# Performance work log

Measured on AMD Instinct MI355X. Metric: run time of the kernel, lower is better.

## Reference

```python
import jax, jax.numpy as jnp
import numpy as np

B, T, L, W = 4, 4096, 64, 8          # batch, text len, media tokens, max_window_per_audio
DIM, DIM_A, H, DH = 2048, 1024, 8, 64
INNER = H * DH
LN_EPS = 1e-5


def setup_inputs() -> dict:
    key = jax.random.key(0)
    ks = jax.random.split(key, 8)
    x = jax.random.normal(ks[0], (B, T, DIM), jnp.float32)
    media = jax.random.normal(ks[1], (B, L, 1, DIM_A), jnp.float32)
    media_mask = jax.random.uniform(ks[2], (B, L, 1)) > 0.1
    # sparse media markers (~8 per row); ensure at least one per row
    media_locations = (jax.random.uniform(ks[3], (B, T)) < (8.0 / T)).astype(jnp.int32)
    media_locations = media_locations.at[:, 0].set(1)
    Wq = jax.random.normal(ks[4], (DIM, INNER), jnp.float32) / np.sqrt(DIM).astype(np.float32)
    Wkv = jax.random.normal(ks[5], (DIM_A, 2 * INNER), jnp.float32) / np.sqrt(DIM_A).astype(np.float32)
    Wout = jax.random.normal(ks[6], (INNER, DIM), jnp.float32) / np.sqrt(INNER).astype(np.float32)
    gamma = jnp.ones((DIM,), jnp.float32)
    beta = jnp.zeros((DIM,), jnp.float32)
    return dict(x=x, media=media, media_mask=media_mask, media_locations=media_locations,
                Wq=Wq, Wkv=Wkv, Wout=Wout, gamma=gamma, beta=beta)


def reference(x, media, media_mask, media_locations, Wq, Wkv, Wout, gamma, beta):
    scale = DH ** -0.5
    # LayerNorm (biased variance, like torch)
    mu = x.mean(-1, keepdims=True)
    var = x.var(-1, keepdims=True)
    xn = (x - mu) * jax.lax.rsqrt(var + LN_EPS) * gamma + beta
    # projections
    q = (xn @ Wq).reshape(B, T, H, DH).transpose(0, 2, 1, 3) * scale   # [B,h,T,dh]
    kv = media.reshape(B, L, DIM_A) @ Wkv
    k, v = jnp.split(kv, 2, axis=-1)
    k = k.reshape(B, L, H, DH).transpose(0, 2, 1, 3)                   # [B,h,L,dh]
    v = v.reshape(B, L, H, DH).transpose(0, 2, 1, 3)
    sim = jnp.einsum('bhid,bhjd->bhij', q, k)                          # [B,h,T,L]
    big = jnp.finfo(sim.dtype).max
    # media validity mask
    mm = media_mask.reshape(B, 1, 1, L)
    sim = jnp.where(mm, sim, -big)
    # few-shot window mask (only_attend_immediate_media=False):
    # token t attends windows [0, max(#media at <=t, 1) * W)
    cum = jnp.cumsum((media_locations != 0).astype(jnp.int32), axis=1)  # [B,T]
    end = jnp.maximum(cum, 1) * W                                       # [B,T]
    fsm = jnp.arange(L)[None, None, :] < end[:, :, None]                # [B,T,L]
    sim = jnp.where(fsm[:, None], sim, -big)
    sim = sim - jax.lax.stop_gradient(sim.max(-1, keepdims=True))
    attn = jax.nn.softmax(sim, axis=-1)
    out = jnp.einsum('bhij,bhjd->bhid', attn, v)                        # [B,h,T,dh]
    out = out.transpose(0, 2, 1, 3).reshape(B, T, INNER)
    return out @ Wout
```

## Files before the change

kernel.cpp:

```cpp
#include <hip/hip_runtime.h>
#include <float.h>

typedef __bf16 bf16;
typedef __bf16 bf16x8 __attribute__((ext_vector_type(8)));
typedef float f32x4 __attribute__((ext_vector_type(4)));

#define GAS __attribute__((address_space(1)))
#define LAS __attribute__((address_space(3)))

__device__ __forceinline__ void gload_lds16(const void* g, void* l) {
  __builtin_amdgcn_global_load_lds((const GAS unsigned int*)g, (LAS unsigned int*)l, 16, 0, 0);
}

template <int OUT_BF16, int BN>
__global__ __launch_bounds__(512, 2) void gemm_pipe(
    const bf16* __restrict__ A, const bf16* __restrict__ Bt,
    void* __restrict__ Cv, int M, int N, int K) {
  constexpr int NR = BN / 64;
  __shared__ __align__(16) bf16 Abuf[4][256 * 32];
  __shared__ __align__(16) bf16 Bbuf[4][BN * 32];
  const int tid = threadIdx.x, lane = tid & 63, w = tid >> 6;
  const int wr = w >> 2, wc = w & 3;
  const int g = lane >> 4, fr = lane & 15;

  const int gx = gridDim.x;
  const int nwg = gx * gridDim.y;
  int lid = blockIdx.y * gx + blockIdx.x;
  {
    const int qq = nwg >> 3, rr = nwg & 7;
    const int xcd = lid & 7, pos = lid >> 3;
    lid = (xcd < rr ? xcd * (qq + 1) : rr * (qq + 1) + (xcd - rr) * qq) + pos;
  }
  const int bx = lid % gx, by = lid / gx;
  const size_t m0 = (size_t)by * 256, n0 = (size_t)bx * BN;

  const int nt = K >> 5;
  const int srow = w * 16 + (lane >> 2);
  const int sdslot = lane & 3;

  auto stageA = [&](int t) {
    const int q = t & 3;
    const int kt = t << 5;
#pragma unroll
    for (int c = 0; c < 2; ++c) {
      const int r = c * 128 + srow;
      const int ss = sdslot ^ ((r >> 1) & 3);
      gload_lds16(A + (m0 + r) * (size_t)K + kt + ss * 8,
                  &Abuf[q][c * 4096 + w * 512]);
    }
  };
  auto stageB = [&](int t) {
    const int q = t & 3;
    const int kt = t << 5;
#pragma unroll
    for (int c = 0; c < BN / 128; ++c) {
      const int r = c * 128 + srow;
      const int ss = sdslot ^ ((r >> 1) & 3);
      gload_lds16(Bt + (n0 + r) * (size_t)K + kt + ss * 8,
                  &Bbuf[q][c * 4096 + w * 512]);
    }
  };
  auto rdA = [&](int q, int mi) {
    const int r = wr * 128 + mi * 16 + fr;
    return *(const bf16x8*)&Abuf[q][r * 32 + ((g ^ ((r >> 1) & 3)) << 3)];
  };
  auto rdB = [&](int q, int ni) {
    const int r = wc * (BN / 4) + ni * 16 + fr;
    return *(const bf16x8*)&Bbuf[q][r * 32 + ((g ^ ((r >> 1) & 3)) << 3)];
  };

  f32x4 acc[8][NR] = {};

#pragma unroll
  for (int t = 0; t < 4; ++t) {
    stageA(t);
    stageB(t);
  }

  const int body = nt - 4;
  for (int t = 0; t < body; ++t) {
    const int q = t & 3;
    if constexpr (BN == 256)
      asm volatile("s_waitcnt vmcnt(12)" ::: "memory");
    else
      asm volatile("s_waitcnt vmcnt(9)" ::: "memory");
    __builtin_amdgcn_s_barrier();
    __builtin_amdgcn_sched_barrier(0);

    bf16x8 bv[NR], av0[4];
#pragma unroll
    for (int ni = 0; ni < NR; ++ni) bv[ni] = rdB(q, ni);
#pragma unroll
    for (int mi = 0; mi < 4; ++mi) av0[mi] = rdA(q, mi);
    __builtin_amdgcn_s_setprio(1);
#pragma unroll
    for (int mi = 0; mi < 4; ++mi)
#pragma unroll
      for (int ni = 0; ni < NR; ++ni)
        acc[mi][ni] = __builtin_amdgcn_mfma_f32_16x16x32_bf16(
            av0[mi], bv[ni], acc[mi][ni], 0, 0, 0);
    __builtin_amdgcn_s_setprio(0);
    __builtin_amdgcn_s_barrier();
    __builtin_amdgcn_sched_barrier(0);
    stageB(t + 4);

    bf16x8 av1[4];
#pragma unroll
    for (int mi = 0; mi < 4; ++mi) av1[mi] = rdA(q, 4 + mi);
    __builtin_amdgcn_s_setprio(1);
#pragma unroll
    for (int mi = 0; mi < 4; ++mi)
#pragma unroll
      for (int ni = 0; ni < NR; ++ni)
        acc[4 + mi][ni] = __builtin_amdgcn_mfma_f32_16x16x32_bf16(
            av1[mi], bv[ni], acc[4 + mi][ni], 0, 0, 0);
    __builtin_amdgcn_s_setprio(0);
    __builtin_amdgcn_s_barrier();
    __builtin_amdgcn_sched_barrier(0);
    stageA(t + 4);
  }

  asm volatile("s_waitcnt vmcnt(0)" ::: "memory");
  __builtin_amdgcn_s_barrier();
  __builtin_amdgcn_sched_barrier(0);
  for (int t = body; t < nt; ++t) {
    const int q = t & 3;
    bf16x8 bv[NR];
#pragma unroll
    for (int ni = 0; ni < NR; ++ni) bv[ni] = rdB(q, ni);
#pragma unroll
    for (int mh = 0; mh < 2; ++mh) {
      bf16x8 av[4];
#pragma unroll
      for (int mi = 0; mi < 4; ++mi) av[mi] = rdA(q, mh * 4 + mi);
#pragma unroll
      for (int mi = 0; mi < 4; ++mi)
#pragma unroll
        for (int ni = 0; ni < NR; ++ni)
          acc[mh * 4 + mi][ni] = __builtin_amdgcn_mfma_f32_16x16x32_bf16(
              av[mi], bv[ni], acc[mh * 4 + mi][ni], 0, 0, 0);
    }
  }

#pragma unroll
  for (int mi = 0; mi < 8; ++mi)
#pragma unroll
    for (int ni = 0; ni < NR; ++ni)
#pragma unroll
      for (int rg = 0; rg < 4; ++rg) {
        const size_t row = m0 + wr * 128 + mi * 16 + g * 4 + rg;
        const size_t col = n0 + wc * (BN / 4) + ni * 16 + fr;
        if (OUT_BF16)
          ((bf16*)Cv)[row * (size_t)N + col] = (bf16)acc[mi][ni][rg];
        else
          ((float*)Cv)[row * (size_t)N + col] = acc[mi][ni][rg];
      }
}

template <int OUT_BF16>
__global__ __launch_bounds__(256, 2) void gemm_bt(
    const bf16* __restrict__ A, const bf16* __restrict__ Bt,
    void* __restrict__ Cv, int M, int N, int K) {
  __shared__ bf16 As[128 * 32];
  __shared__ bf16 Bs[128 * 32];
  const int tid = threadIdx.x;
  const int lane = tid & 63, w = tid >> 6;
  const int wr = w >> 1, wc = w & 1;

  const int gx = gridDim.x;
  const int nwg = gx * gridDim.y;
  int lid = blockIdx.y * gx + blockIdx.x;
  {
    const int qq = nwg >> 3, rr = nwg & 7;
    const int xcd = lid & 7, pos = lid >> 3;
    lid = (xcd < rr ? xcd * (qq + 1) : rr * (qq + 1) + (xcd - rr) * qq) + pos;
  }
  const int bx = lid % gx, by = lid / gx;
  const size_t m0 = (size_t)by * 128, n0 = (size_t)bx * 128;

  const int srow = lane >> 2, sslot = lane & 3;
  const int g = lane >> 4, fr = lane & 15;

  f32x4 acc[4][4] = {};

  for (int kt = 0; kt < K; kt += 32) {
    __syncthreads();
#pragma unroll
    for (int j = 0; j < 2; ++j) {
      const int c = 2 * w + j;
      const int r = c * 16 + srow;
      const int ks = (sslot ^ (r & 3)) << 3;
      gload_lds16(A + (m0 + r) * K + kt + ks, &As[c * 512]);
      gload_lds16(Bt + (n0 + r) * K + kt + ks, &Bs[c * 512]);
    }
    __syncthreads();
    bf16x8 av[4], bv[4];
#pragma unroll
    for (int mi = 0; mi < 4; ++mi) {
      const int r = wr * 64 + mi * 16 + fr;
      av[mi] = *(const bf16x8*)&As[r * 32 + ((g ^ (r & 3)) << 3)];
    }
#pragma unroll
    for (int ni = 0; ni < 4; ++ni) {
      const int r = wc * 64 + ni * 16 + fr;
      bv[ni] = *(const bf16x8*)&Bs[r * 32 + ((g ^ (r & 3)) << 3)];
    }
#pragma unroll
    for (int mi = 0; mi < 4; ++mi)
#pragma unroll
      for (int ni = 0; ni < 4; ++ni)
        acc[mi][ni] = __builtin_amdgcn_mfma_f32_16x16x32_bf16(
            av[mi], bv[ni], acc[mi][ni], 0, 0, 0);
  }

#pragma unroll
  for (int mi = 0; mi < 4; ++mi)
#pragma unroll
    for (int ni = 0; ni < 4; ++ni)
#pragma unroll
      for (int rg = 0; rg < 4; ++rg) {
        const size_t row = m0 + wr * 64 + mi * 16 + g * 4 + rg;
        const size_t col = n0 + wc * 64 + ni * 16 + fr;
        if (OUT_BF16)
          ((bf16*)Cv)[row * (size_t)N + col] = (bf16)acc[mi][ni][rg];
        else
          ((float*)Cv)[row * (size_t)N + col] = acc[mi][ni][rg];
      }
}

__device__ __forceinline__ void transp64(const float* __restrict__ src,
                                         bf16* __restrict__ dst, int R, int C,
                                         float scale, int tile, float* lds) {
  const int tilesC = C >> 6;
  const int tr = tile / tilesC, tc = tile % tilesC;
  const int r0 = tr << 6, c0 = tc << 6;
  const int tid = threadIdx.x;
  const int lr = tid >> 6, lc = tid & 63;
#pragma unroll
  for (int j = 0; j < 16; ++j) {
    const int r = j * 4 + lr;
    lds[r * 65 + lc] = src[(size_t)(r0 + r) * C + c0 + lc];
  }
  __syncthreads();
#pragma unroll
  for (int j = 0; j < 16; ++j) {
    const int rr = j * 4 + lr;
    dst[(size_t)(c0 + rr) * R + r0 + lc] = (bf16)(lds[lc * 65 + rr] * scale);
  }
}

__global__ __launch_bounds__(256) void prep_all(
    const float* __restrict__ x, const float* __restrict__ gamma,
    const float* __restrict__ beta, bf16* __restrict__ xn,
    const float* __restrict__ Wq, bf16* __restrict__ wqT,
    const float* __restrict__ Wkv, bf16* __restrict__ wkvT,
    const float* __restrict__ Wout, bf16* __restrict__ woT,
    const float* __restrict__ media, bf16* __restrict__ medb,
    const int* __restrict__ mloc, int* __restrict__ endw,
    const unsigned char* __restrict__ mraw, int* __restrict__ mk) {
  __shared__ float shf[64 * 65];
  const int blk = blockIdx.x, tid = threadIdx.x;

  if (blk < 16384) {
    const size_t base = (size_t)blk * 2048 + tid * 8;
    f32x4 v0 = *(const f32x4*)(x + base);
    f32x4 v1 = *(const f32x4*)(x + base + 4);
    float s = 0.f, q2 = 0.f;
#pragma unroll
    for (int j = 0; j < 4; ++j) {
      s += v0[j] + v1[j];
      q2 += v0[j] * v0[j] + v1[j] * v1[j];
    }
    for (int off = 32; off > 0; off >>= 1) {
      s += __shfl_down(s, off);
      q2 += __shfl_down(q2, off);
    }
    const int lane = tid & 63, wv = tid >> 6;
    if (lane == 0) { shf[wv] = s; shf[4 + wv] = q2; }
    __syncthreads();
    s = shf[0] + shf[1] + shf[2] + shf[3];
    q2 = shf[4] + shf[5] + shf[6] + shf[7];
    const float mu = s * (1.f / 2048.f);
    const float var = q2 * (1.f / 2048.f) - mu * mu;
    const float rs = rsqrtf(var + 1e-5f);
    f32x4 g0 = *(const f32x4*)(gamma + tid * 8);
    f32x4 g1 = *(const f32x4*)(gamma + tid * 8 + 4);
    f32x4 b0 = *(const f32x4*)(beta + tid * 8);
    f32x4 b1 = *(const f32x4*)(beta + tid * 8 + 4);
    bf16x8 o;
#pragma unroll
    for (int j = 0; j < 4; ++j) {
      o[j] = (bf16)((v0[j] - mu) * rs * g0[j] + b0[j]);
      o[4 + j] = (bf16)((v1[j] - mu) * rs * g1[j] + b1[j]);
    }
    *(bf16x8*)(xn + base) = o;
  } else if (blk < 16640) {
    transp64(Wq, wqT, 2048, 512, 0.125f, blk - 16384, shf);
  } else if (blk < 16896) {
    transp64(Wkv, wkvT, 1024, 1024, 1.f, blk - 16640, shf);
  } else if (blk < 17152) {
    transp64(Wout, woT, 512, 2048, 1.f, blk - 16896, shf);
  } else if (blk < 18176) {
    const int i = (blk - 17152) * 256 + tid;
    medb[i] = (bf16)media[i];
  } else if (blk < 18180) {
    int* part = (int*)shf;
    const int b = blk - 18176;
    int loc[16];
    int s = 0;
    const int base = b * 4096 + tid * 16;
#pragma unroll
    for (int j = 0; j < 16; ++j) {
      loc[j] = (mloc[base + j] != 0) ? 1 : 0;
      s += loc[j];
    }
    part[tid] = s;
    __syncthreads();
    for (int off = 1; off < 256; off <<= 1) {
      int v = (tid >= off) ? part[tid - off] : 0;
      __syncthreads();
      part[tid] += v;
      __syncthreads();
    }
    int c = (tid > 0) ? part[tid - 1] : 0;
#pragma unroll
    for (int j = 0; j < 16; ++j) {
      c += loc[j];
      int e = (c > 1 ? c : 1) << 3;
      endw[base + j] = e > 64 ? 64 : e;
    }
  } else {
    int* isbool = (int*)shf;
    if (tid == 0) *isbool = 0;
    __syncthreads();
    const unsigned char v = mraw[tid];
    if ((tid & 3) != 0 && v != 0) atomicOr(isbool, 1);
    __syncthreads();
    mk[tid] = (*isbool) ? (int)mraw[tid] : ((const int*)mraw)[tid];
  }
}

__global__ __launch_bounds__(256, 2) void attn_kernel(
    const bf16* __restrict__ q, const bf16* __restrict__ kv,
    const int* __restrict__ mk, const int* __restrict__ endw,
    bf16* __restrict__ ao) {
  __shared__ bf16 Ks[64 * 64], Vs[64 * 64], Ps[64 * 64];
  __shared__ int mks[64];
  const int tid = threadIdx.x, lane = tid & 63, w = tid >> 6;
  const int b = blockIdx.z, h = blockIdx.y, t0 = blockIdx.x * 64;

#pragma unroll
  for (int s0 = 0; s0 < 2; ++s0) {
    const int sidx = s0 * 256 + tid;
    const int r = sidx >> 3, sl = sidx & 7;
    *(bf16x8*)&Ks[r * 64 + ((sl ^ (r & 7)) << 3)] =
        *(const bf16x8*)&kv[(size_t)(b * 64 + r) * 1024 + h * 64 + sl * 8];
    bf16x8 vv =
        *(const bf16x8*)&kv[(size_t)(b * 64 + r) * 1024 + 512 + h * 64 + sl * 8];
#pragma unroll
    for (int j = 0; j < 8; ++j) {
      const int dh = sl * 8 + j;
      Vs[dh * 64 + ((((r >> 3) ^ (dh & 7)) << 3) | (r & 7))] = vv[j];
    }
  }
  if (tid < 64) mks[tid] = mk[b * 64 + tid];
  __syncthreads();

  const int g = lane >> 4, fr = lane & 15;
  bf16x8 aq[2];
#pragma unroll
  for (int kg = 0; kg < 2; ++kg)
    aq[kg] = *(const bf16x8*)&q[(size_t)(b * 4096 + t0 + w * 16 + fr) * 512 +
                                h * 64 + kg * 32 + g * 8];
  f32x4 sacc[4] = {};
#pragma unroll
  for (int kg = 0; kg < 2; ++kg)
#pragma unroll
    for (int ni = 0; ni < 4; ++ni) {
      const int r = ni * 16 + fr;
      bf16x8 bk = *(const bf16x8*)&Ks[r * 64 + (((kg * 4 + g) ^ (r & 7)) << 3)];
      sacc[ni] = __builtin_amdgcn_mfma_f32_16x16x32_bf16(aq[kg], bk, sacc[ni],
                                                         0, 0, 0);
    }

  const int4 ev4 = *(const int4*)&endw[b * 4096 + t0 + w * 16 + g * 4];
  const int ev[4] = {ev4.x, ev4.y, ev4.z, ev4.w};
  float p[4][4];
#pragma unroll
  for (int ni = 0; ni < 4; ++ni) {
    const int l = ni * 16 + fr;
    const bool mv = (mks[l] != 0);
#pragma unroll
    for (int rg = 0; rg < 4; ++rg)
      p[ni][rg] = (mv && (l < ev[rg])) ? sacc[ni][rg] : -FLT_MAX;
  }
#pragma unroll
  for (int rg = 0; rg < 4; ++rg) {
    float m = fmaxf(fmaxf(p[0][rg], p[1][rg]), fmaxf(p[2][rg], p[3][rg]));
    m = fmaxf(m, __shfl_xor(m, 1));
    m = fmaxf(m, __shfl_xor(m, 2));
    m = fmaxf(m, __shfl_xor(m, 4));
    m = fmaxf(m, __shfl_xor(m, 8));
    float sum = 0.f;
#pragma unroll
    for (int ni = 0; ni < 4; ++ni) {
      p[ni][rg] = __expf(p[ni][rg] - m);
      sum += p[ni][rg];
    }
    sum += __shfl_xor(sum, 1);
    sum += __shfl_xor(sum, 2);
    sum += __shfl_xor(sum, 4);
    sum += __shfl_xor(sum, 8);
    const float inv = 1.f / sum;
#pragma unroll
    for (int ni = 0; ni < 4; ++ni) p[ni][rg] *= inv;
  }
#pragma unroll
  for (int ni = 0; ni < 4; ++ni) {
    const int l = ni * 16 + fr;
#pragma unroll
    for (int rg = 0; rg < 4; ++rg) {
      const int tr = w * 16 + g * 4 + rg;
      Ps[tr * 64 + ((((l >> 3) ^ (tr & 7)) << 3) | (l & 7))] = (bf16)p[ni][rg];
    }
  }
  __syncthreads();

  bf16x8 pa[2];
#pragma unroll
  for (int kg = 0; kg < 2; ++kg) {
    const int r = w * 16 + fr;
    pa[kg] = *(const bf16x8*)&Ps[r * 64 + (((kg * 4 + g) ^ (r & 7)) << 3)];
  }
  f32x4 oacc[4] = {};
#pragma unroll
  for (int kg = 0; kg < 2; ++kg)
#pragma unroll
    for (int ni = 0; ni < 4; ++ni) {
      const int r = ni * 16 + fr;
      bf16x8 bv = *(const bf16x8*)&Vs[r * 64 + (((kg * 4 + g) ^ (r & 7)) << 3)];
      oacc[ni] = __builtin_amdgcn_mfma_f32_16x16x32_bf16(pa[kg], bv, oacc[ni],
                                                         0, 0, 0);
    }
#pragma unroll
  for (int ni = 0; ni < 4; ++ni)
#pragma unroll
    for (int rg = 0; rg < 4; ++rg)
      ao[(size_t)(b * 4096 + t0 + w * 16 + g * 4 + rg) * 512 + h * 64 +
         ni * 16 + fr] = (bf16)oacc[ni][rg];
}

extern "C" void kernel_launch(void* const* d_in, const int* in_sizes, int n_in,
                              void* d_out, int out_size, void* d_ws,
                              size_t ws_size, hipStream_t stream) {
  const float* x = (const float*)d_in[0];
  const float* media = (const float*)d_in[1];
  const unsigned char* mraw = (const unsigned char*)d_in[2];
  const int* mloc = (const int*)d_in[3];
  const float* Wq = (const float*)d_in[4];
  const float* Wkv = (const float*)d_in[5];
  const float* Wout = (const float*)d_in[6];
  const float* gamma = (const float*)d_in[7];
  const float* beta = (const float*)d_in[8];
  float* out = (float*)d_out;

  bf16* xn = (bf16*)d_out;

  char* ws = (char*)d_ws;
  size_t off = 0;
  auto carve = [&](size_t bytes) {
    void* p = ws + off;
    off += (bytes + 255) & ~(size_t)255;
    return p;
  };
  bf16* qb = (bf16*)carve((size_t)16384 * 512 * 2);
  bf16* aob = (bf16*)carve((size_t)16384 * 512 * 2);
  bf16* kvb = (bf16*)carve((size_t)256 * 1024 * 2);
  bf16* wqT = (bf16*)carve((size_t)512 * 2048 * 2);
  bf16* wkvT = (bf16*)carve((size_t)1024 * 1024 * 2);
  bf16* woT = (bf16*)carve((size_t)2048 * 512 * 2);
  bf16* medb = (bf16*)carve((size_t)256 * 1024 * 2);
  int* endw = (int*)carve((size_t)4 * 4096 * 4);
  int* mk = (int*)carve(256 * 4);
  (void)ws_size;
  (void)in_sizes;
  (void)n_in;
  (void)out_size;

  prep_all<<<18181, 256, 0, stream>>>(x, gamma, beta, xn, Wq, wqT, Wkv, wkvT,
                                      Wout, woT, media, medb, mloc, endw, mraw,
                                      mk);

  gemm_bt<1><<<dim3(8, 2), 256, 0, stream>>>(medb, wkvT, kvb, 256, 1024, 1024);

  gemm_pipe<1, 128><<<dim3(4, 64), 512, 0, stream>>>(xn, wqT, qb, 16384, 512,
                                                     2048);

  attn_kernel<<<dim3(64, 8, 4), 256, 0, stream>>>(qb, kvb, mk, endw, aob);

  gemm_pipe<0, 256><<<dim3(8, 64), 512, 0, stream>>>(aob, woT, out, 16384,
                                                     2048, 512);
}
```

Baseline: 193.3 us.

## Replace GEMM pipeline with 3-stage K=64 tiling and fixed 256x128 tiles

Replaces the templated 4-buffer K=32 GEMM, which staged A and B separately with split barriers, by a single 256x128 tile GEMM. It uses a 3-stage LDS ring with K=64 slices and an XOR swizzle over 8 slots, and issues one stage per iteration before computing. The aim is fewer barriers and waits per unit of K and longer MFMA bursts. The output projection now uses 128-wide N tiles on a 16x64 grid instead of 256-wide tiles, so there are more workgroups but less B reuse per tile. LDS use rises to about 144KB, which may limit occupancy to one block per CU despite launch bounds of 2.

```diff
diff --git a/kernel.cpp b/kernel.cpp
--- a/kernel.cpp
+++ b/kernel.cpp
@@ -12,15 +12,14 @@
   __builtin_amdgcn_global_load_lds((const GAS unsigned int*)g, (LAS unsigned int*)l, 16, 0, 0);
 }
 
-template <int OUT_BF16, int BN>
-__global__ __launch_bounds__(512, 2) void gemm_pipe(
+template <int OUT_BF16>
+__global__ __launch_bounds__(512, 2) void gemm_big(
     const bf16* __restrict__ A, const bf16* __restrict__ Bt,
     void* __restrict__ Cv, int M, int N, int K) {
-  constexpr int NR = BN / 64;
-  __shared__ __align__(16) bf16 Abuf[4][256 * 32];
-  __shared__ __align__(16) bf16 Bbuf[4][BN * 32];
-  const int tid = threadIdx.x, lane = tid & 63, w = tid >> 6;
-  const int wr = w >> 2, wc = w & 3;
+  __shared__ __align__(16) bf16 Abuf[3][256 * 64];
+  __shared__ __align__(16) bf16 Bbuf[3][128 * 64];
+  const int tid = threadIdx.x, lane = tid & 63;
+  const int w = tid >> 6, wr = w >> 2, wc = w & 3;
   const int g = lane >> 4, fr = lane & 15;
 
   const int gx = gridDim.x;
@@ -32,124 +31,86 @@
     lid = (xcd < rr ? xcd * (qq + 1) : rr * (qq + 1) + (xcd - rr) * qq) + pos;
   }
   const int bx = lid % gx, by = lid / gx;
-  const size_t m0 = (size_t)by * 256, n0 = (size_t)bx * BN;
-
-  const int nt = K >> 5;
-  const int srow = w * 16 + (lane >> 2);
-  const int sdslot = lane & 3;
-
-  auto stageA = [&](int t) {
-    const int q = t & 3;
-    const int kt = t << 5;
+  const size_t m0 = (size_t)by * 256, n0 = (size_t)bx * 128;
+
+  const int nt = K >> 6;
+  const int srow = tid >> 3;
+  const int sslot = tid & 7;
+
+  f32x4 acc[8][2] = {};
+
+  auto stage = [&](int t) {
+    const int s = t % 3;
+    const int kt = t << 6;
+#pragma unroll
+    for (int c = 0; c < 4; ++c) {
+      const int r = c * 64 + srow;
+      gload_lds16(A + (m0 + r) * (size_t)K + kt + ((sslot ^ (r & 7)) << 3),
+                  &Abuf[s][c * 4096 + w * 512]);
+    }
 #pragma unroll
     for (int c = 0; c < 2; ++c) {
-      const int r = c * 128 + srow;
-      const int ss = sdslot ^ ((r >> 1) & 3);
-      gload_lds16(A + (m0 + r) * (size_t)K + kt + ss * 8,
-                  &Abuf[q][c * 4096 + w * 512]);
+      const int r = c * 64 + srow;
+      gload_lds16(Bt + (n0 + r) * (size_t)K + kt + ((sslot ^ (r & 7)) << 3),
+                  &Bbuf[s][c * 4096 + w * 512]);
     }
   };
-  auto stageB = [&](int t) {
-    const int q = t & 3;
-    const int kt = t << 5;
-#pragma unroll
-    for (int c = 0; c < BN / 128; ++c) {
-      const int r = c * 128 + srow;
-      const int ss = sdslot ^ ((r >> 1) & 3);
-      gload_lds16(Bt + (n0 + r) * (size_t)K + kt + ss * 8,
-                  &Bbuf[q][c * 4096 + w * 512]);
-    }
+
+  auto rdA = [&](int s, int mi, int ks) {
+    const int r = wr * 128 + mi * 16 + fr;
+    return *(const bf16x8*)&Abuf[s][r * 64 + ((((ks << 2) | g) ^ (r & 7)) << 3)];
   };
-  auto rdA = [&](int q, int mi) {
-    const int r = wr * 128 + mi * 16 + fr;
-    return *(const bf16x8*)&Abuf[q][r * 32 + ((g ^ ((r >> 1) & 3)) << 3)];
+  auto rdB = [&](int s, int ni, int ks) {
+    const int r = wc * 32 + ni * 16 + fr;
+    return *(const bf16x8*)&Bbuf[s][r * 64 + ((((ks << 2) | g) ^ (r & 7)) << 3)];
   };
-  auto rdB = [&](int q, int ni) {
-    const int r = wc * (BN / 4) + ni * 16 + fr;
-    return *(const bf16x8*)&Bbuf[q][r * 32 + ((g ^ ((r >> 1) & 3)) << 3)];
+
+  auto compute = [&](int t) {
+    const int s = t % 3;
+    bf16x8 bv[2][2];
+#pragma unroll
+    for (int ni = 0; ni < 2; ++ni)
+#pragma unroll
+      for (int ks = 0; ks < 2; ++ks) bv[ni][ks] = rdB(s, ni, ks);
+    __builtin_amdgcn_s_setprio(1);
+#pragma unroll
+    for (int mi = 0; mi < 8; ++mi)
+#pragma unroll
+      for (int ks = 0; ks < 2; ++ks) {
+        const bf16x8 av = rdA(s, mi, ks);
+#pragma unroll
+        for (int ni = 0; ni < 2; ++ni)
+          acc[mi][ni] = __builtin_amdgcn_mfma_f32_16x16x32_bf16(
+              av, bv[ni][ks], acc[mi][ni], 0, 0, 0);
+      }
+    __builtin_amdgcn_s_setprio(0);
   };
 
-  f32x4 acc[8][NR] = {};
-
-#pragma unroll
-  for (int t = 0; t < 4; ++t) {
-    stageA(t);
-    stageB(t);
-  }
-
-  const int body = nt - 4;
-  for (int t = 0; t < body; ++t) {
-    const int q = t & 3;
-    if constexpr (BN == 256)
-      asm volatile("s_waitcnt vmcnt(12)" ::: "memory");
-    else
-      asm volatile("s_waitcnt vmcnt(9)" ::: "memory");
+  stage(0);
+  stage(1);
+
+  for (int t = 0; t < nt - 1; ++t) {
+    __builtin_amdgcn_sched_barrier(0);
+    asm volatile("s_waitcnt vmcnt(6)" ::: "memory");
     __builtin_amdgcn_s_barrier();
     __builtin_amdgcn_sched_barrier(0);
-
-    bf16x8 bv[NR], av0[4];
-#pragma unroll
-    for (int ni = 0; ni < NR; ++ni) bv[ni] = rdB(q, ni);
-#pragma unroll
-    for (int mi = 0; mi < 4; ++mi) av0[mi] = rdA(q, mi);
-    __builtin_amdgcn_s_setprio(1);
-#pragma unroll
-    for (int mi = 0; mi < 4; ++mi)
-#pragma unroll
-      for (int ni = 0; ni < NR; ++ni)
-        acc[mi][ni] = __builtin_amdgcn_mfma_f32_16x16x32_bf16(
-            av0[mi], bv[ni], acc[mi][ni], 0, 0, 0);
-    __builtin_amdgcn_s_setprio(0);
-    __builtin_amdgcn_s_barrier();
-    __builtin_amdgcn_sched_barrier(0);
-    stageB(t + 4);
-
-    bf16x8 av1[4];
-#pragma unroll
-    for (int mi = 0; mi < 4; ++mi) av1[mi] = rdA(q, 4 + mi);
-    __builtin_amdgcn_s_setprio(1);
-#pragma unroll
-    for (int mi = 0; mi < 4; ++mi)
-#pragma unroll
-      for (int ni = 0; ni < NR; ++ni)
-        acc[4 + mi][ni] = __builtin_amdgcn_mfma_f32_16x16x32_bf16(
-            av1[mi], bv[ni], acc[4 + mi][ni], 0, 0, 0);
-    __builtin_amdgcn_s_setprio(0);
-    __builtin_amdgcn_s_barrier();
-    __builtin_amdgcn_sched_barrier(0);
-    stageA(t + 4);
-  }
-
+    if (t + 2 < nt) stage(t + 2);
+    compute(t);
+  }
+  __builtin_amdgcn_sched_barrier(0);
   asm volatile("s_waitcnt vmcnt(0)" ::: "memory");
   __builtin_amdgcn_s_barrier();
   __builtin_amdgcn_sched_barrier(0);
-  for (int t = body; t < nt; ++t) {
-    const int q = t & 3;
-    bf16x8 bv[NR];
-#pragma unroll
-    for (int ni = 0; ni < NR; ++ni) bv[ni] = rdB(q, ni);
-#pragma unroll
-    for (int mh = 0; mh < 2; ++mh) {
-      bf16x8 av[4];
-#pragma unroll
-      for (int mi = 0; mi < 4; ++mi) av[mi] = rdA(q, mh * 4 + mi);
-#pragma unroll
-      for (int mi = 0; mi < 4; ++mi)
-#pragma unroll
-        for (int ni = 0; ni < NR; ++ni)
-          acc[mh * 4 + mi][ni] = __builtin_amdgcn_mfma_f32_16x16x32_bf16(
-              av[mi], bv[ni], acc[mh * 4 + mi][ni], 0, 0, 0);
-    }
-  }
+  compute(nt - 1);
 
 #pragma unroll
   for (int mi = 0; mi < 8; ++mi)
 #pragma unroll
-    for (int ni = 0; ni < NR; ++ni)
+    for (int ni = 0; ni < 2; ++ni)
 #pragma unroll
       for (int rg = 0; rg < 4; ++rg) {
         const size_t row = m0 + wr * 128 + mi * 16 + g * 4 + rg;
-        const size_t col = n0 + wc * (BN / 4) + ni * 16 + fr;
+        const size_t col = n0 + wc * 32 + ni * 16 + fr;
         if (OUT_BF16)
           ((bf16*)Cv)[row * (size_t)N + col] = (bf16)acc[mi][ni][rg];
         else
@@ -493,11 +454,10 @@
 
   gemm_bt<1><<<dim3(8, 2), 256, 0, stream>>>(medb, wkvT, kvb, 256, 1024, 1024);
 
-  gemm_pipe<1, 128><<<dim3(4, 64), 512, 0, stream>>>(xn, wqT, qb, 16384, 512,
-                                                     2048);
+  gemm_big<1><<<dim3(4, 64), 512, 0, stream>>>(xn, wqT, qb, 16384, 512, 2048);
 
   attn_kernel<<<dim3(64, 8, 4), 256, 0, stream>>>(qb, kvb, mk, endw, aob);
 
-  gemm_pipe<0, 256><<<dim3(8, 64), 512, 0, stream>>>(aob, woT, out, 16384,
-                                                     2048, 512);
-}
+  gemm_big<0><<<dim3(16, 64), 512, 0, stream>>>(aob, woT, out, 16384, 2048,
+                                                512);
+}
```

Measured after the change: 182.4 us. -5.6%, faster.
